# Kernel optimization log

Measured on AMD Instinct MI355X. Metric: run time of the kernel, lower is better.

The kernel has to match this reference:

```python
import jax, jax.numpy as jnp
import numpy as np
from jax.scipy.special import digamma, polygamma

N_ITERS = 100
TOL = 1e-3


def setup_inputs() -> dict:
    key = jax.random.key(0)
    x = jax.random.normal(key, (2_000_000, 10), dtype=jnp.float32)
    return {"x": x}


def reference(x):
    # x: [n, C] logits -> Dirichlet MLE over softmax probabilities
    p = jax.nn.softmax(x, axis=-1)            # [n, C]
    n = p.shape[0]
    m1 = p.mean(0)                            # [C] E[p]
    m2 = (p ** 2).mean(0)                     # [C] E[p^2]
    # method-of-moments initialization (as in the torch module)
    a0 = m1 * ((m1 - m2) / (m2 - m1 ** 2)).mean(-1)
    # loop-invariant sufficient statistic
    log_p_avg = jnp.log(p).mean(0)            # [C]

    def cond(carry):
        a, k, diff = carry
        return jnp.logical_and(k < N_ITERS, diff >= TOL)

    def body(carry):
        a, k, _ = carry
        g = (digamma(a.sum(-1)) - digamma(a) + log_p_avg) * n
        q = -n * polygamma(1, a)
        z = n * polygamma(1, a.sum(-1))
        q_inv = 1.0 / q
        b = (g * q_inv).sum(-1) / (1.0 / z + q_inv.sum(-1))
        a_new = a - (g - b) / q               # Newton step with rank-1 Hessian inverse
        diff = jnp.abs(a_new - a).sum()       # L1 norm, matches torch.norm(.,1)
        return (a_new, k + 1, diff)

    a, _, _ = jax.lax.while_loop(
        cond, body, (a0, jnp.int32(0), jnp.float32(jnp.inf))
    )
    return a.astype(jnp.float32)
```

## Files before the change

kernel.cpp:

```cpp
#include <hip/hip_runtime.h>
#include <math.h>

#define C 10
#define BLOCK 256
#define NBLOCKS 1024
#define TILE_ROWS 512
#define TILE_ELEMS (TILE_ROWS * C)
#define NSTATS (3 * C)



__device__ __forceinline__ void accum_row(const float* __restrict__ row,
                                          float* __restrict__ s1,
                                          float* __restrict__ s2,
                                          float* __restrict__ sl) {
  float v[C];
#pragma unroll
  for (int c = 0; c < C; c++) v[c] = row[c];
  float mx = v[0];
#pragma unroll
  for (int c = 1; c < C; c++) mx = fmaxf(mx, v[c]);
  float e[C], se = 0.f;
#pragma unroll
  for (int c = 0; c < C; c++) { v[c] -= mx; e[c] = __expf(v[c]); se += e[c]; }
  float inv = 1.0f / se;
  float lse = __logf(se);
#pragma unroll
  for (int c = 0; c < C; c++) {
    float p = e[c] * inv;
    s1[c] += p;
    s2[c] = fmaf(p, p, s2[c]);
    sl[c] += v[c] - lse;
  }
}


__device__ __forceinline__ void digtri8(double x, double& dg, double& tg) {
  double i0 = 1.0 / x,        i1 = 1.0 / (x + 1.0);
  double i2 = 1.0 / (x + 2.0), i3 = 1.0 / (x + 3.0);
  double i4 = 1.0 / (x + 4.0), i5 = 1.0 / (x + 5.0);
  double i6 = 1.0 / (x + 6.0), i7 = 1.0 / (x + 7.0);
  double rd = (i0 + i1) + (i2 + i3) + ((i4 + i5) + (i6 + i7));
  double rt = (i0 * i0 + i1 * i1) + (i2 * i2 + i3 * i3) +
              ((i4 * i4 + i5 * i5) + (i6 * i6 + i7 * i7));
  double y = x + 8.0;
  double yi = 1.0 / y, f = yi * yi;
  dg = log(y) - 0.5 * yi
     - f * (1.0 / 12 - f * (1.0 / 120 - f * (1.0 / 252 - f * (1.0 / 240 - f * (1.0 / 132)))))
     - rd;
  tg = rt + yi + 0.5 * f
     + f * yi * (1.0 / 6 - f * (1.0 / 30 - f * (1.0 / 42 - f * (1.0 / 30))));
}

__device__ __forceinline__ double wsum16(double v) {
#pragma unroll
  for (int off = 1; off < 16; off <<= 1) v += __shfl_xor(v, off);
  return v;
}


__global__ __launch_bounds__(BLOCK) void dir_fused_kernel(
    const float* __restrict__ x, unsigned* __restrict__ counter,
    double* __restrict__ sums, float* __restrict__ out,
    int nrows, int ntiles, int tailStart, int nblocks) {
  __shared__ float tile[TILE_ELEMS];
  __shared__ float red[4][NSTATS];
  __shared__ int lastFlag;
  const int tid = threadIdx.x;

  float s1[C], s2[C], sl[C];
#pragma unroll
  for (int c = 0; c < C; c++) { s1[c] = 0.f; s2[c] = 0.f; sl[c] = 0.f; }

  for (int t = blockIdx.x; t < ntiles; t += nblocks) {
    const float4* __restrict__ src = (const float4*)(x + (size_t)t * TILE_ELEMS);
    float4* dst = (float4*)tile;
#pragma unroll
    for (int i = 0; i < TILE_ELEMS / 4 / BLOCK; i++)
      dst[tid + i * BLOCK] = src[tid + i * BLOCK];
    __syncthreads();
#pragma unroll
    for (int r = 0; r < TILE_ROWS / BLOCK; r++)
      accum_row(tile + (size_t)(r * BLOCK + tid) * C, s1, s2, sl);
    __syncthreads();
  }

  if (blockIdx.x == nblocks - 1) {
    for (int rr = tailStart + tid; rr < nrows; rr += BLOCK)
      accum_row(x + (size_t)rr * C, s1, s2, sl);
  }

  const int lane = tid & 63;
  const int wave = tid >> 6;
#pragma unroll
  for (int c = 0; c < C; c++) {
    float v1 = s1[c], v2 = s2[c], v3 = sl[c];
#pragma unroll
    for (int off = 32; off >= 1; off >>= 1) {
      v1 += __shfl_down(v1, off);
      v2 += __shfl_down(v2, off);
      v3 += __shfl_down(v3, off);
    }
    if (lane == 0) {
      red[wave][c] = v1;
      red[wave][C + c] = v2;
      red[wave][2 * C + c] = v3;
    }
  }
  __syncthreads();
  if (tid < NSTATS) {
    float tot = red[0][tid] + red[1][tid] + red[2][tid] + red[3][tid];
    atomicAdd(&sums[tid], (double)tot);
  }
  __syncthreads();
  if (tid == 0) {
    __threadfence();
    unsigned old = atomicAdd(counter, 1u);
    lastFlag = (old == (unsigned)(nblocks - 1)) ? 1 : 0;
  }
  __syncthreads();
  if (!lastFlag) return;

  if (tid < 16) {
    const int c = tid;
    const bool act = (c < C);
    const double n = (double)nrows;
    double m1 = 0.0, m2 = 0.0, lpa = 0.0;
    if (act) {
      m1  = __hip_atomic_load(&sums[c],         __ATOMIC_RELAXED, __HIP_MEMORY_SCOPE_AGENT) / n;
      m2  = __hip_atomic_load(&sums[C + c],     __ATOMIC_RELAXED, __HIP_MEMORY_SCOPE_AGENT) / n;
      lpa = __hip_atomic_load(&sums[2 * C + c], __ATOMIC_RELAXED, __HIP_MEMORY_SCOPE_AGENT) / n;
    }
    double ratio = act ? (m1 - m2) / (m2 - m1 * m1) : 0.0;
    double rmean = wsum16(ratio) / (double)C;
    double a = act ? m1 * rmean : 0.0;

    double diff = 1e30;
    for (int k = 0; k < 100 && diff >= 1e-3; k++) {
      double S = wsum16(a);
      double dgl, tgl;
      digtri8(act ? a : S, dgl, tgl);
      double dgS = __shfl(dgl, 10);
      double tgS = __shfl(tgl, 10);
      double g = act ? (dgS - dgl + lpa) * n : 0.0;
      double qinv = act ? (-1.0) / (n * tgl) : 0.0;
      double z = n * tgS;
      double num = wsum16(g * qinv);
      double den = 1.0 / z + wsum16(qinv);
      double b = num / den;
      double anew = act ? a - (g - b) * qinv : 0.0;
      diff = wsum16(fabs(anew - a));
      a = anew;
    }
    if (act) out[c] = (float)a;
  }
}


extern "C" void kernel_launch(void* const* d_in, const int* in_sizes, int n_in,
                              void* d_out, int out_size, void* d_ws, size_t ws_size,
                              hipStream_t stream) {
  const float* x = (const float*)d_in[0];
  const int total = in_sizes[0];
  const int nrows = total / C;
  const int ntiles = nrows / TILE_ROWS;
  const int tailStart = ntiles * TILE_ROWS;

  unsigned* counter = (unsigned*)d_ws;
  double* sums = (double*)((char*)d_ws + 64);

  hipMemsetAsync(d_ws, 0, 512, stream);
  dir_fused_kernel<<<NBLOCKS, BLOCK, 0, stream>>>(
      x, counter, sums, (float*)d_out, nrows, ntiles, tailStart, NBLOCKS);
}
```

Measured before the change: 144.1 us.

## Replace global double atomics with per-block partials and double the grid

Each block now writes its 30 partial sums to a per-block slot in workspace instead of doing double-precision atomicAdds on 30 shared addresses. The last block then reduces all partials in double before running the Newton iterations. The grid doubles to 2048 blocks, and each tile shrinks to 256 rows so a thread handles one row per tile. This is meant to remove atomic contention and raise parallelism, at the cost of a serial final reduction over all partials in the last block and more tile barriers.

```diff
diff --git a/kernel.cpp b/kernel.cpp
--- a/kernel.cpp
+++ b/kernel.cpp
@@ -3,9 +3,10 @@
 
 #define C 10
 #define BLOCK 256
-#define NBLOCKS 1024
-#define TILE_ROWS 512
+#define NBLOCKS 2048
+#define TILE_ROWS 256
 #define TILE_ELEMS (TILE_ROWS * C)
+#define NF4 (TILE_ELEMS / 4)
 #define NSTATS (3 * C)
 
 
@@ -36,7 +37,7 @@
 
 
 __device__ __forceinline__ void digtri8(double x, double& dg, double& tg) {
-  double i0 = 1.0 / x,        i1 = 1.0 / (x + 1.0);
+  double i0 = 1.0 / x,         i1 = 1.0 / (x + 1.0);
   double i2 = 1.0 / (x + 2.0), i3 = 1.0 / (x + 3.0);
   double i4 = 1.0 / (x + 4.0), i5 = 1.0 / (x + 5.0);
   double i6 = 1.0 / (x + 6.0), i7 = 1.0 / (x + 7.0);
@@ -61,10 +62,11 @@
 
 __global__ __launch_bounds__(BLOCK) void dir_fused_kernel(
     const float* __restrict__ x, unsigned* __restrict__ counter,
-    double* __restrict__ sums, float* __restrict__ out,
+    float* __restrict__ partials, float* __restrict__ out,
     int nrows, int ntiles, int tailStart, int nblocks) {
   __shared__ float tile[TILE_ELEMS];
   __shared__ float red[4][NSTATS];
+  __shared__ double tot[NSTATS];
   __shared__ int lastFlag;
   const int tid = threadIdx.x;
 
@@ -76,12 +78,10 @@
     const float4* __restrict__ src = (const float4*)(x + (size_t)t * TILE_ELEMS);
     float4* dst = (float4*)tile;
 #pragma unroll
-    for (int i = 0; i < TILE_ELEMS / 4 / BLOCK; i++)
-      dst[tid + i * BLOCK] = src[tid + i * BLOCK];
+    for (int i = tid; i < NF4; i += BLOCK)
+      dst[i] = src[i];
     __syncthreads();
-#pragma unroll
-    for (int r = 0; r < TILE_ROWS / BLOCK; r++)
-      accum_row(tile + (size_t)(r * BLOCK + tid) * C, s1, s2, sl);
+    accum_row(tile + (size_t)tid * C, s1, s2, sl);
     __syncthreads();
   }
 
@@ -109,8 +109,8 @@
   }
   __syncthreads();
   if (tid < NSTATS) {
-    float tot = red[0][tid] + red[1][tid] + red[2][tid] + red[3][tid];
-    atomicAdd(&sums[tid], (double)tot);
+    float totf = red[0][tid] + red[1][tid] + red[2][tid] + red[3][tid];
+    partials[(size_t)tid * nblocks + blockIdx.x] = totf;
   }
   __syncthreads();
   if (tid == 0) {
@@ -121,15 +121,31 @@
   __syncthreads();
   if (!lastFlag) return;
 
+  {
+    const int j = tid >> 3;
+    const int k = tid & 7;
+    double s = 0.0;
+    if (j < NSTATS) {
+      const float* __restrict__ base = partials + (size_t)j * nblocks;
+#pragma unroll 16
+      for (int b = k; b < nblocks; b += 8)
+        s += (double)__hip_atomic_load(&base[b], __ATOMIC_RELAXED, __HIP_MEMORY_SCOPE_AGENT);
+    }
+#pragma unroll
+    for (int off = 1; off < 8; off <<= 1) s += __shfl_xor(s, off);
+    if (j < NSTATS && k == 0) tot[j] = s;
+  }
+  __syncthreads();
+
   if (tid < 16) {
     const int c = tid;
     const bool act = (c < C);
     const double n = (double)nrows;
     double m1 = 0.0, m2 = 0.0, lpa = 0.0;
     if (act) {
-      m1  = __hip_atomic_load(&sums[c],         __ATOMIC_RELAXED, __HIP_MEMORY_SCOPE_AGENT) / n;
-      m2  = __hip_atomic_load(&sums[C + c],     __ATOMIC_RELAXED, __HIP_MEMORY_SCOPE_AGENT) / n;
-      lpa = __hip_atomic_load(&sums[2 * C + c], __ATOMIC_RELAXED, __HIP_MEMORY_SCOPE_AGENT) / n;
+      m1 = tot[c] / n;
+      m2 = tot[C + c] / n;
+      lpa = tot[2 * C + c] / n;
     }
     double ratio = act ? (m1 - m2) / (m2 - m1 * m1) : 0.0;
     double rmean = wsum16(ratio) / (double)C;
@@ -166,10 +182,17 @@
   const int ntiles = nrows / TILE_ROWS;
   const int tailStart = ntiles * TILE_ROWS;
 
+  int grid = NBLOCKS;
+  size_t need = 256 + (size_t)NSTATS * grid * sizeof(float);
+  if (need > ws_size) {
+    grid = (int)((ws_size - 256) / (NSTATS * sizeof(float)));
+    if (grid < 1) grid = 1;
+  }
+
   unsigned* counter = (unsigned*)d_ws;
-  double* sums = (double*)((char*)d_ws + 64);
+  float* partials = (float*)((char*)d_ws + 256);
 
-  hipMemsetAsync(d_ws, 0, 512, stream);
-  dir_fused_kernel<<<NBLOCKS, BLOCK, 0, stream>>>(
-      x, counter, sums, (float*)d_out, nrows, ntiles, tailStart, NBLOCKS);
+  hipMemsetAsync(d_ws, 0, 256, stream);
+  dir_fused_kernel<<<grid, BLOCK, 0, stream>>>(
+      x, counter, partials, (float*)d_out, nrows, ntiles, tailStart, grid);
 }
```

Result: slower. 181.2 us (+25.8%).
